# Kernel tuning notes

Measured on AMD Instinct MI355X. Metric: run time of the kernel, lower is better.

## Reference

```python
import jax, jax.numpy as jnp
import numpy as np

EMBED_DIM = 1024
SEQ_LEN = 4096
NUM_HEADS = 16
HEAD_DIM = EMBED_DIM // NUM_HEADS
FREQ_BINS = SEQ_LEN // 2 + 1  # 2049
LN_EPS = 1e-5


def setup_inputs() -> dict:
    key = jax.random.key(0)
    ks = jax.random.split(key, 12)
    B = 4
    x = jax.random.normal(ks[0], (B, SEQ_LEN, EMBED_DIM), dtype=jnp.float32)
    # LayerNorm affine params
    ln_w = jnp.ones((EMBED_DIM,), dtype=jnp.float32)
    ln_b = jnp.zeros((EMBED_DIM,), dtype=jnp.float32)
    # spectral base filter / bias: (H, freq_bins, 1)
    base_filter = jax.random.normal(ks[1], (NUM_HEADS, FREQ_BINS, 1), dtype=jnp.float32)
    base_bias = jax.random.normal(ks[2], (NUM_HEADS, FREQ_BINS, 1), dtype=jnp.float32) - 0.1
    # adaptive MLP (depth=2, width=embed_dim): D -> D -> D -> H*freq*2, relu hidden
    out_size = NUM_HEADS * FREQ_BINS * 2
    s0 = 1.0 / np.sqrt(EMBED_DIM)
    w0 = jax.random.uniform(ks[3], (EMBED_DIM, EMBED_DIM), jnp.float32, -s0, s0)
    b0 = jax.random.uniform(ks[4], (EMBED_DIM,), jnp.float32, -s0, s0)
    w1 = jax.random.uniform(ks[5], (EMBED_DIM, EMBED_DIM), jnp.float32, -s0, s0)
    b1 = jax.random.uniform(ks[6], (EMBED_DIM,), jnp.float32, -s0, s0)
    w2 = jax.random.uniform(ks[7], (EMBED_DIM, out_size), jnp.float32, -s0, s0)
    b2 = jax.random.uniform(ks[8], (out_size,), jnp.float32, -s0, s0)
    return {"x": x, "ln_w": ln_w, "ln_b": ln_b,
            "base_filter": base_filter, "base_bias": base_bias,
            "w0": w0, "b0": b0, "w1": w1, "b1": b1, "w2": w2, "b2": b2}


def _complex_activation(z):
    mag = jnp.abs(z)
    scale = jax.nn.gelu(mag) / (mag + 1e-6)
    return z * scale


def reference(x, ln_w, ln_b, base_filter, base_bias, w0, b0, w1, b1, w2, b2):
    B, N, D = x.shape  # N == SEQ_LEN, D == EMBED_DIM
    # pre-norm LayerNorm over last dim
    mu = x.mean(axis=-1, keepdims=True)
    var = x.var(axis=-1, keepdims=True)
    x_norm = (x - mu) / jnp.sqrt(var + LN_EPS) * ln_w + ln_b
    # split heads: (B, H, N, head_dim)
    x_heads = x_norm.reshape(B, N, NUM_HEADS, HEAD_DIM).transpose(0, 2, 1, 3)
    F_fft = jnp.fft.rfft(x_heads, axis=2)  # (B, H, freq, head_dim), complex
    # adaptive params from mean-pooled context
    context = x_norm.mean(axis=1)  # (B, D)
    h = jax.nn.relu(context @ w0 + b0)
    h = jax.nn.relu(h @ w1 + b1)
    adapt = h @ w2 + b2  # (B, H*freq*2)
    adapt = adapt.reshape(B, NUM_HEADS, FREQ_BINS, 2)
    adaptive_scale = adapt[..., 0:1]
    adaptive_bias = adapt[..., 1:2]
    effective_filter = base_filter * (1.0 + adaptive_scale)  # (B, H, freq, 1)
    effective_bias = base_bias + adaptive_bias
    F_mod = F_fft * effective_filter + effective_bias
    F_nl = _complex_activation(F_mod)
    x_filt = jnp.fft.irfft(F_nl, n=SEQ_LEN, axis=2)  # (B, H, N, head_dim)
    x_filt = x_filt.transpose(0, 2, 1, 3).reshape(B, SEQ_LEN, EMBED_DIM)
    return x_filt  # dropout is identity (inference / rate 0)
```

## Files before the change

kernel.cpp:

```cpp
#include <hip/hip_runtime.h>
#include <hip/hip_fp16.h>
#include <math.h>

#define B_ 4
#define N_ 4096
#define D_ 1024
#define H_ 16
#define HD_ 64
#define FB_ 2049

typedef unsigned short ushort_t;
typedef unsigned int uint_t;

__device__ __forceinline__ float2 cmul(float2 a, float2 b) {
    return make_float2(a.x*b.x - a.y*b.y, a.x*b.y + a.y*b.x);
}
__device__ __forceinline__ float2 cadd(float2 a, float2 b){return make_float2(a.x+b.x,a.y+b.y);}
__device__ __forceinline__ float2 csub(float2 a, float2 b){return make_float2(a.x-b.x,a.y-b.y);}
__device__ __forceinline__ float2 cconj(float2 a){return make_float2(a.x,-a.y);}
__device__ __forceinline__ float2 addi(float2 a, float2 b){return make_float2(a.x-b.y, a.y+b.x);}
__device__ __forceinline__ float2 subi(float2 a, float2 b){return make_float2(a.x+b.y, a.y-b.x);}

__device__ __forceinline__ float gelu_t(float m) {
    float u = 0.7978845608028654f * (m + 0.044715f * m * m * m);
    float e = __expf(-2.0f * u);
    float th = (1.0f - e) / (1.0f + e);
    return 0.5f * m * (1.0f + th);
}
__device__ __forceinline__ float2 cact(float2 z) {
    float m = sqrtf(z.x*z.x + z.y*z.y);
    float s = gelu_t(m) / (m + 1e-6f);
    return make_float2(z.x*s, z.y*s);
}

__device__ __forceinline__ ushort_t f2h(float f) {
    __half h = __float2half_rn(f);
    return *reinterpret_cast<ushort_t*>(&h);
}
__device__ __forceinline__ float h2f(ushort_t u) {
    __half h = *reinterpret_cast<__half*>(&u);
    return __half2float(h);
}
__device__ __forceinline__ uint_t pk2(float a, float b) {
    return (uint_t)f2h(a) | ((uint_t)f2h(b) << 16);
}
__device__ __forceinline__ float lo_f(uint_t u){ return h2f((ushort_t)(u & 0xffffu)); }
__device__ __forceinline__ float hi_f(uint_t u){ return h2f((ushort_t)(u >> 16)); }

#define IX(e) ((e) + ((e) >> 4))

__global__ __launch_bounds__(256) void k_normT(const float* __restrict__ x,
                                               const float* __restrict__ lnw,
                                               const float* __restrict__ lnb,
                                               ushort_t* __restrict__ xt,
                                               float* __restrict__ cpart) {
    __shared__ ushort_t lds16[32 * 1032];
    uint_t* lds32 = (uint_t*)lds16;
    int blk = blockIdx.x;
    int b = blk >> 7, chunk = blk & 127;
    int n0 = chunk << 5;
    int lane = threadIdx.x & 63, w = threadIdx.x >> 6;
    const float4* lw4 = (const float4*)lnw;
    const float4* lb4 = (const float4*)lnb;
    float4 W0 = lw4[lane], W1 = lw4[lane+64], W2 = lw4[lane+128], W3 = lw4[lane+192];
    float4 G0 = lb4[lane], G1 = lb4[lane+64], G2 = lb4[lane+128], G3 = lb4[lane+192];

    for (int j = 0; j < 8; j++) {
        int r = (w << 3) + j;
        const float4* xr = (const float4*)(x + ((size_t)b * N_ + n0 + r) * D_);
        float4 v0 = xr[lane], v1 = xr[lane+64], v2 = xr[lane+128], v3 = xr[lane+192];
        float s = v0.x+v0.y+v0.z+v0.w + v1.x+v1.y+v1.z+v1.w
                + v2.x+v2.y+v2.z+v2.w + v3.x+v3.y+v3.z+v3.w;
        float q = v0.x*v0.x+v0.y*v0.y+v0.z*v0.z+v0.w*v0.w
                + v1.x*v1.x+v1.y*v1.y+v1.z*v1.z+v1.w*v1.w
                + v2.x*v2.x+v2.y*v2.y+v2.z*v2.z+v2.w*v2.w
                + v3.x*v3.x+v3.y*v3.y+v3.z*v3.z+v3.w*v3.w;
        for (int o = 1; o < 64; o <<= 1) { s += __shfl_xor(s, o); q += __shfl_xor(q, o); }
        float mu = s * (1.0f / D_);
        float rstd = rsqrtf(q * (1.0f / D_) - mu * mu + 1e-5f);
        int base = r * 516 + 2 * lane;
        lds32[base]       = pk2((v0.x-mu)*rstd*W0.x+G0.x, (v0.y-mu)*rstd*W0.y+G0.y);
        lds32[base + 1]   = pk2((v0.z-mu)*rstd*W0.z+G0.z, (v0.w-mu)*rstd*W0.w+G0.w);
        lds32[base + 128] = pk2((v1.x-mu)*rstd*W1.x+G1.x, (v1.y-mu)*rstd*W1.y+G1.y);
        lds32[base + 129] = pk2((v1.z-mu)*rstd*W1.z+G1.z, (v1.w-mu)*rstd*W1.w+G1.w);
        lds32[base + 256] = pk2((v2.x-mu)*rstd*W2.x+G2.x, (v2.y-mu)*rstd*W2.y+G2.y);
        lds32[base + 257] = pk2((v2.z-mu)*rstd*W2.z+G2.z, (v2.w-mu)*rstd*W2.w+G2.w);
        lds32[base + 384] = pk2((v3.x-mu)*rstd*W3.x+G3.x, (v3.y-mu)*rstd*W3.y+G3.y);
        lds32[base + 385] = pk2((v3.z-mu)*rstd*W3.z+G3.z, (v3.w-mu)*rstd*W3.w+G3.w);
    }
    __syncthreads();
    for (int dd = 0; dd < 4; dd++) {
        int d = threadIdx.x + (dd << 8);
        float cs = 0.f;
        uint_t u[16];
        #pragma unroll
        for (int i = 0; i < 16; i++) {
            ushort_t h0 = lds16[(2*i) * 1032 + d];
            ushort_t h1 = lds16[(2*i+1) * 1032 + d];
            cs += h2f(h0) + h2f(h1);
            u[i] = (uint_t)h0 | ((uint_t)h1 << 16);
        }
        uint4* dst = (uint4*)(xt + ((size_t)(b * 1024 + d)) * 4096 + n0);
        dst[0] = make_uint4(u[0], u[1], u[2], u[3]);
        dst[1] = make_uint4(u[4], u[5], u[6], u[7]);
        dst[2] = make_uint4(u[8], u[9], u[10], u[11]);
        dst[3] = make_uint4(u[12], u[13], u[14], u[15]);
        cpart[((size_t)(b * 128 + chunk)) * D_ + d] = cs;
    }
}

__global__ __launch_bounds__(256) void k_ctx(const float* __restrict__ cpart,
                                             float* __restrict__ ctx) {
    int id = blockIdx.x * 256 + threadIdx.x;
    int b = id >> 10, d = id & 1023;
    float s = 0.f;
    const float* p = cpart + (size_t)b * 128 * D_ + d;
    #pragma unroll 8
    for (int g = 0; g < 128; g++) s += p[g * D_];
    ctx[id] = s * (1.0f / N_);
}

__global__ __launch_bounds__(256) void k_mlp_part(const float* __restrict__ in,
                                                  const float* __restrict__ w,
                                                  float* __restrict__ part) {
    __shared__ float li[4 * 256];
    int ks = blockIdx.y;
    for (int i = threadIdx.x; i < 1024; i += 256) {
        int b = i >> 8, kk = i & 255;
        li[i] = in[b * 1024 + ks * 256 + kk];
    }
    __syncthreads();
    int col = blockIdx.x * 64 + (threadIdx.x & 63);
    int b = threadIdx.x >> 6;
    const float* wp = w + (size_t)(ks * 256) * 1024 + col;
    const float* ip = li + b * 256;
    float acc = 0.f;
    #pragma unroll 8
    for (int k = 0; k < 256; k++) acc = fmaf(ip[k], wp[(size_t)k * 1024], acc);
    part[((size_t)ks * 4 + b) * 1024 + col] = acc;
}

__global__ __launch_bounds__(256) void k_mlp_part2(const float* __restrict__ part,
                                                   const float* __restrict__ bias,
                                                   const float* __restrict__ w,
                                                   float* __restrict__ part2) {
    __shared__ float li[4 * 256];
    int ks = blockIdx.y;
    for (int i = threadIdx.x; i < 1024; i += 256) {
        int b = i >> 8, kk = (i & 255) + ks * 256;
        float v = part[b * 1024 + kk] + part[4096 + b * 1024 + kk] +
                  part[8192 + b * 1024 + kk] + part[12288 + b * 1024 + kk] + bias[kk];
        li[i] = fmaxf(v, 0.f);
    }
    __syncthreads();
    int col = blockIdx.x * 64 + (threadIdx.x & 63);
    int b = threadIdx.x >> 6;
    const float* wp = w + (size_t)(ks * 256) * 1024 + col;
    const float* ip = li + b * 256;
    float acc = 0.f;
    #pragma unroll 8
    for (int k = 0; k < 256; k++) acc = fmaf(ip[k], wp[(size_t)k * 1024], acc);
    part2[((size_t)ks * 4 + b) * 1024 + col] = acc;
}

__global__ __launch_bounds__(256) void k_adapt_part(const float* __restrict__ part2,
                                                    const float* __restrict__ b1,
                                                    const float* __restrict__ w2,
                                                    float* __restrict__ part3) {
    __shared__ float lh[4 * 128];
    int ks = blockIdx.y;
    for (int i = threadIdx.x; i < 512; i += 256) {
        int b = i >> 7, kk = (i & 127) + ks * 128;
        float v = part2[b * 1024 + kk] + part2[4096 + b * 1024 + kk] +
                  part2[8192 + b * 1024 + kk] + part2[12288 + b * 1024 + kk] + b1[kk];
        lh[i] = fmaxf(v, 0.f);
    }
    __syncthreads();
    int j4 = blockIdx.x * 1024 + threadIdx.x * 4;
    if (j4 < 65568) {
        float a0x=0,a0y=0,a0z=0,a0w=0, a1x=0,a1y=0,a1z=0,a1w=0;
        float a2x=0,a2y=0,a2z=0,a2w=0, a3x=0,a3y=0,a3z=0,a3w=0;
        const float* wp = w2 + (size_t)(ks * 128) * 65568 + j4;
        #pragma unroll 4
        for (int k = 0; k < 128; k++) {
            float4 wv = *(const float4*)(wp + (size_t)k * 65568);
            float h0 = lh[k], h1 = lh[128 + k], h2 = lh[256 + k], h3 = lh[384 + k];
            a0x = fmaf(h0, wv.x, a0x); a0y = fmaf(h0, wv.y, a0y);
            a0z = fmaf(h0, wv.z, a0z); a0w = fmaf(h0, wv.w, a0w);
            a1x = fmaf(h1, wv.x, a1x); a1y = fmaf(h1, wv.y, a1y);
            a1z = fmaf(h1, wv.z, a1z); a1w = fmaf(h1, wv.w, a1w);
            a2x = fmaf(h2, wv.x, a2x); a2y = fmaf(h2, wv.y, a2y);
            a2z = fmaf(h2, wv.z, a2z); a2w = fmaf(h2, wv.w, a2w);
            a3x = fmaf(h3, wv.x, a3x); a3y = fmaf(h3, wv.y, a3y);
            a3z = fmaf(h3, wv.z, a3z); a3w = fmaf(h3, wv.w, a3w);
        }
        float* p3 = part3 + (size_t)ks * 4 * 65568 + j4;
        *(float4*)(p3)              = make_float4(a0x, a0y, a0z, a0w);
        *(float4*)(p3 + 65568)      = make_float4(a1x, a1y, a1z, a1w);
        *(float4*)(p3 + 2 * 65568)  = make_float4(a2x, a2y, a2z, a2w);
        *(float4*)(p3 + 3 * 65568)  = make_float4(a3x, a3y, a3z, a3w);
    }
}

__global__ __launch_bounds__(256) void k_eff(const float* __restrict__ part3,
                                             const float* __restrict__ b2,
                                             const float* __restrict__ bfilt,
                                             const float* __restrict__ bbias,
                                             float2* __restrict__ eff) {
    int p = blockIdx.x * 256 + threadIdx.x;
    if (p >= 32784) return;
    int h = p / 2049, f = p % 2049;
    float bf = bfilt[p], bb = bbias[p];
    float sc0 = b2[2 * p], bi0 = b2[2 * p + 1];
    #pragma unroll
    for (int b = 0; b < 4; b++) {
        float sc = sc0, bi = bi0;
        #pragma unroll
        for (int s = 0; s < 8; s++) {
            const float* q = part3 + ((size_t)s * 4 + b) * 65568 + 2 * p;
            sc += q[0]; bi += q[1];
        }
        eff[((size_t)b * H_ + h) * FB_ + f] = make_float2(bf * (1.0f + sc), bb + bi);
    }
}

__global__ __launch_bounds__(512) void k_fftmod(ushort_t* __restrict__ xt,
                                                const float2* __restrict__ eff) {
    __shared__ float2 bufA[4352];
    __shared__ float2 bufB[4352];
    __shared__ float2 tw[1088];
    const float s2 = 0.70710678118654752f;
    int t = threadIdx.x;
    int sig0 = blockIdx.x * 2;
    int b = sig0 >> 10;
    int h = (sig0 & 1023) >> 6;
    const float2* ef = eff + ((size_t)b * H_ + h) * FB_;
    ushort_t* xs = xt + (size_t)sig0 * 4096;

    #pragma unroll
    for (int ii = 0; ii < 2; ii++) {
        int ji = t + ii * 512;
        float sv, cv;
        __sincosf(-(float)M_PI * (float)ji * (1.0f / 2048.0f), &sv, &cv);
        tw[IX(ji)] = make_float2(cv, sv);
    }
    {
        const uint4* pa = (const uint4*)xs;
        const uint4* pb = pa + 512;
        uint4 ua = pa[t], ub = pb[t];
        int n = t << 3;
        bufA[IX(n+0)] = make_float2(lo_f(ua.x), lo_f(ub.x));
        bufA[IX(n+1)] = make_float2(hi_f(ua.x), hi_f(ub.x));
        bufA[IX(n+2)] = make_float2(lo_f(ua.y), lo_f(ub.y));
        bufA[IX(n+3)] = make_float2(hi_f(ua.y), hi_f(ub.y));
        bufA[IX(n+4)] = make_float2(lo_f(ua.z), lo_f(ub.z));
        bufA[IX(n+5)] = make_float2(hi_f(ua.z), hi_f(ub.z));
        bufA[IX(n+6)] = make_float2(lo_f(ua.w), lo_f(ub.w));
        bufA[IX(n+7)] = make_float2(hi_f(ua.w), hi_f(ub.w));
    }
    __syncthreads();

    float2 *src = bufA, *dst = bufB;
    for (int m = 1; m <= 512; m <<= 3) {
        int idx = t;
        int km = idx & (m - 1);
        int jm = idx - km;
        float2 u0 = src[IX(idx)];
        float2 u1 = src[IX(idx + 512)];
        float2 u2 = src[IX(idx + 1024)];
        float2 u3 = src[IX(idx + 1536)];
        float2 u4 = src[IX(idx + 2048)];
        float2 u5 = src[IX(idx + 2560)];
        float2 u6 = src[IX(idx + 3072)];
        float2 u7 = src[IX(idx + 3584)];
        float2 a0 = cadd(u0,u4), a1 = csub(u0,u4), a2 = cadd(u2,u6), a3 = csub(u2,u6);
        float2 E0 = cadd(a0,a2), E1 = subi(a1,a3), E2 = csub(a0,a2), E3 = addi(a1,a3);
        float2 c0 = cadd(u1,u5), c1 = csub(u1,u5), c2 = cadd(u3,u7), c3 = csub(u3,u7);
        float2 O0 = cadd(c0,c2), O1 = subi(c1,c3), O2 = csub(c0,c2), O3 = addi(c1,c3);
        float2 R1 = make_float2(s2*(O1.x + O1.y), s2*(O1.y - O1.x));
        float2 R2 = make_float2(O2.y, -O2.x);
        float2 R3 = make_float2(s2*(O3.y - O3.x), -s2*(O3.x + O3.y));
        float2 X0 = cadd(E0,O0), X4 = csub(E0,O0);
        float2 X1 = cadd(E1,R1), X5 = csub(E1,R1);
        float2 X2 = cadd(E2,R2), X6 = csub(E2,R2);
        float2 X3 = cadd(E3,R3), X7 = csub(E3,R3);
        float2 w1 = tw[IX(jm)];
        float2 w2 = cmul(w1,w1), w3 = cmul(w2,w1), w4 = cmul(w2,w2);
        float2 w5 = cmul(w4,w1), w6 = cmul(w4,w2), w7 = cmul(w4,w3);
        int base = 8*idx - 7*km;
        dst[IX(base)]       = X0;
        dst[IX(base + m)]   = cmul(w1,X1);
        dst[IX(base + 2*m)] = cmul(w2,X2);
        dst[IX(base + 3*m)] = cmul(w3,X3);
        dst[IX(base + 4*m)] = cmul(w4,X4);
        dst[IX(base + 5*m)] = cmul(w5,X5);
        dst[IX(base + 6*m)] = cmul(w6,X6);
        dst[IX(base + 7*m)] = cmul(w7,X7);
        __syncthreads();
        float2* tmp = src; src = dst; dst = tmp;
    }

    if (t == 0) {
        float2 Z = src[IX(0)];
        float2 e0 = ef[0];
        float Av = Z.x * e0.x + e0.y;
        float Bv = Z.y * e0.x + e0.y;
        float ma = fabsf(Av); Av *= gelu_t(ma) / (ma + 1e-6f);
        float mb = fabsf(Bv); Bv *= gelu_t(mb) / (mb + 1e-6f);
        dst[IX(0)] = make_float2(Av, Bv);
    }
    #pragma unroll
    for (int ii = 0; ii < 4; ii++) {
        int k = 1 + t + ii * 512;
        if (k == 2048) {
            float2 Z = src[IX(2048)];
            float2 eN = ef[2048];
            float Av = Z.x * eN.x + eN.y;
            float Bv = Z.y * eN.x + eN.y;
            float ma = fabsf(Av); Av *= gelu_t(ma) / (ma + 1e-6f);
            float mb = fabsf(Bv); Bv *= gelu_t(mb) / (mb + 1e-6f);
            dst[IX(2048)] = make_float2(Av, Bv);
        } else {
            float2 Zk = src[IX(k)], Zq = src[IX(4096 - k)];
            float2 A  = make_float2(0.5f*(Zk.x + Zq.x), 0.5f*(Zk.y - Zq.y));
            float2 Bc = make_float2(0.5f*(Zk.y + Zq.y), 0.5f*(Zq.x - Zk.x));
            float2 e = ef[k];
            float2 Ap = make_float2(A.x * e.x + e.y,  A.y * e.x);
            float2 Bp = make_float2(Bc.x * e.x + e.y, Bc.y * e.x);
            Ap = cact(Ap); Bp = cact(Bp);
            dst[IX(k)]        = make_float2(Ap.x - Bp.y, Ap.y + Bp.x);
            dst[IX(4096 - k)] = make_float2(Ap.x + Bp.y, Bp.x - Ap.y);
        }
    }
    __syncthreads();
    { float2* tmp = src; src = dst; dst = tmp; }

    for (int m = 1; m <= 512; m <<= 3) {
        int idx = t;
        int km = idx & (m - 1);
        int jm = idx - km;
        float2 u0 = src[IX(idx)];
        float2 u1 = src[IX(idx + 512)];
        float2 u2 = src[IX(idx + 1024)];
        float2 u3 = src[IX(idx + 1536)];
        float2 u4 = src[IX(idx + 2048)];
        float2 u5 = src[IX(idx + 2560)];
        float2 u6 = src[IX(idx + 3072)];
        float2 u7 = src[IX(idx + 3584)];
        float2 a0 = cadd(u0,u4), a1 = csub(u0,u4), a2 = cadd(u2,u6), a3 = csub(u2,u6);
        float2 E0 = cadd(a0,a2), E1 = addi(a1,a3), E2 = csub(a0,a2), E3 = subi(a1,a3);
        float2 c0 = cadd(u1,u5), c1 = csub(u1,u5), c2 = cadd(u3,u7), c3 = csub(u3,u7);
        float2 O0 = cadd(c0,c2), O1 = addi(c1,c3), O2 = csub(c0,c2), O3 = subi(c1,c3);
        float2 R1 = make_float2(s2*(O1.x - O1.y),  s2*(O1.x + O1.y));
        float2 R2 = make_float2(-O2.y, O2.x);
        float2 R3 = make_float2(-s2*(O3.x + O3.y), s2*(O3.x - O3.y));
        float2 X0 = cadd(E0,O0), X4 = csub(E0,O0);
        float2 X1 = cadd(E1,R1), X5 = csub(E1,R1);
        float2 X2 = cadd(E2,R2), X6 = csub(E2,R2);
        float2 X3 = cadd(E3,R3), X7 = csub(E3,R3);
        float2 w1 = cconj(tw[IX(jm)]);
        float2 w2 = cmul(w1,w1), w3 = cmul(w2,w1), w4 = cmul(w2,w2);
        float2 w5 = cmul(w4,w1), w6 = cmul(w4,w2), w7 = cmul(w4,w3);
        int base = 8*idx - 7*km;
        dst[IX(base)]       = X0;
        dst[IX(base + m)]   = cmul(w1,X1);
        dst[IX(base + 2*m)] = cmul(w2,X2);
        dst[IX(base + 3*m)] = cmul(w3,X3);
        dst[IX(base + 4*m)] = cmul(w4,X4);
        dst[IX(base + 5*m)] = cmul(w5,X5);
        dst[IX(base + 6*m)] = cmul(w6,X6);
        dst[IX(base + 7*m)] = cmul(w7,X7);
        __syncthreads();
        float2* tmp = src; src = dst; dst = tmp;
    }

    {
        const float sc = 1.0f / 4096.0f;
        int n = t << 3;
        float2 z0 = src[IX(n+0)], z1 = src[IX(n+1)], z2 = src[IX(n+2)], z3 = src[IX(n+3)];
        float2 z4 = src[IX(n+4)], z5 = src[IX(n+5)], z6 = src[IX(n+6)], z7 = src[IX(n+7)];
        uint4 oa, ob;
        oa.x = pk2(z0.x*sc, z1.x*sc); oa.y = pk2(z2.x*sc, z3.x*sc);
        oa.z = pk2(z4.x*sc, z5.x*sc); oa.w = pk2(z6.x*sc, z7.x*sc);
        ob.x = pk2(z0.y*sc, z1.y*sc); ob.y = pk2(z2.y*sc, z3.y*sc);
        ob.z = pk2(z4.y*sc, z5.y*sc); ob.w = pk2(z6.y*sc, z7.y*sc);
        ((uint4*)xs)[t] = oa;
        ((uint4*)xs)[t + 512] = ob;
    }
}

__global__ __launch_bounds__(256) void k_transout(const ushort_t* __restrict__ xt,
                                                  float* __restrict__ out) {
    __shared__ float tile[64 * 65];
    int bid = blockIdx.x;
    int b = bid >> 10;
    int rem = bid & 1023;
    int nt = rem >> 4;
    int dt = rem & 15;
    int n0 = nt << 6;
    int tx = threadIdx.x & 63, ty = threadIdx.x >> 6;
    const ushort_t* xtb = xt + ((size_t)((b * H_ + dt) * HD_)) * (size_t)N_ + n0;
    for (int r = 0; r < 16; r++) {
        int dloc = ty + 4 * r;
        tile[dloc * 65 + tx] = h2f(xtb[(size_t)dloc * N_ + tx]);
    }
    __syncthreads();
    float* ob = out + ((size_t)b * N_ + n0) * D_ + dt * HD_;
    for (int r = 0; r < 16; r++) {
        int nn = ty + 4 * r;
        ob[(size_t)nn * D_ + tx] = tile[tx * 65 + nn];
    }
}

extern "C" void kernel_launch(void* const* d_in, const int* in_sizes, int n_in,
                              void* d_out, int out_size, void* d_ws, size_t ws_size,
                              hipStream_t stream) {
    const float* x     = (const float*)d_in[0];
    const float* lnw   = (const float*)d_in[1];
    const float* lnb   = (const float*)d_in[2];
    const float* bfilt = (const float*)d_in[3];
    const float* bbias = (const float*)d_in[4];
    const float* w0    = (const float*)d_in[5];
    const float* b0    = (const float*)d_in[6];
    const float* w1    = (const float*)d_in[7];
    const float* b1    = (const float*)d_in[8];
    const float* w2    = (const float*)d_in[9];
    const float* b2    = (const float*)d_in[10];

    float* ws = (float*)d_ws;
    ushort_t* xt   = (ushort_t*)ws;
    float*  cpart  = ws + 8388608;
    float*  ctx    = ws + 8912896;
    float*  pA     = ws + 8916992;
    float*  pB     = ws + 8933376;
    float*  p3     = ws + 8949760;
    float2* eff    = (float2*)(ws + 11047936);
    float*  out    = (float*)d_out;

    k_normT     <<<512,  256, 0, stream>>>(x, lnw, lnb, xt, cpart);
    k_ctx       <<<16,   256, 0, stream>>>(cpart, ctx);
    k_mlp_part  <<<dim3(16, 4), 256, 0, stream>>>(ctx, w0, pA);
    k_mlp_part2 <<<dim3(16, 4), 256, 0, stream>>>(pA, b0, w1, pB);
    k_adapt_part<<<dim3(65, 8), 256, 0, stream>>>(pB, b1, w2, p3);
    k_eff       <<<129,  256, 0, stream>>>(p3, b2, bfilt, bbias, eff);
    k_fftmod    <<<2048, 512, 0, stream>>>(xt, eff);
    k_transout  <<<4096, 256, 0, stream>>>(xt, out);
}
```

Baseline: 227.4 us.

## Use in-place DIF/DIT FFT with digit-reversed spectrum and single LDS buffer

Replaces the ping-pong Stockham FFT with in-place decimation-in-frequency forward and decimation-in-time inverse radix-8 stages. The spectrum is left in digit-reversed order and the modulation step indexes it through rev12, so one LDS buffer is enough and the twiddle table is halved. The intent is to cut LDS use per block so more blocks fit per CU, with launch bounds now asking for 6 blocks per CU, and to skip twiddles in the trivial stage. The normT transpose also reads packed 32-bit LDS words and writes two columns per thread. Risks are bank conflicts from the strided in-place access and precision drift from computing twiddle powers by repeated multiplication.

```diff
diff --git a/kernel.cpp b/kernel.cpp
--- a/kernel.cpp
+++ b/kernel.cpp
@@ -48,6 +48,10 @@
 __device__ __forceinline__ float hi_f(uint_t u){ return h2f((ushort_t)(u >> 16)); }
 
 #define IX(e) ((e) + ((e) >> 4))
+
+__device__ __forceinline__ int rev12(int p) {
+    return ((p & 7) << 9) | (((p >> 3) & 7) << 6) | (((p >> 6) & 7) << 3) | ((p >> 9) & 7);
+}
 
 __global__ __launch_bounds__(256) void k_normT(const float* __restrict__ x,
                                                const float* __restrict__ lnw,
@@ -89,23 +93,31 @@
         lds32[base + 385] = pk2((v3.z-mu)*rstd*W3.z+G3.z, (v3.w-mu)*rstd*W3.w+G3.w);
     }
     __syncthreads();
-    for (int dd = 0; dd < 4; dd++) {
-        int d = threadIdx.x + (dd << 8);
-        float cs = 0.f;
-        uint_t u[16];
+    for (int half = 0; half < 2; half++) {
+        int dp = threadIdx.x + (half << 8);
+        float cs_e = 0.f, cs_o = 0.f;
+        uint_t ce[16], co[16];
         #pragma unroll
         for (int i = 0; i < 16; i++) {
-            ushort_t h0 = lds16[(2*i) * 1032 + d];
-            ushort_t h1 = lds16[(2*i+1) * 1032 + d];
-            cs += h2f(h0) + h2f(h1);
-            u[i] = (uint_t)h0 | ((uint_t)h1 << 16);
+            uint_t w0 = lds32[(2*i) * 516 + dp];
+            uint_t w1 = lds32[(2*i+1) * 516 + dp];
+            ce[i] = (w0 & 0xffffu) | (w1 << 16);
+            co[i] = (w0 >> 16) | (w1 & 0xffff0000u);
+            cs_e += lo_f(w0) + lo_f(w1);
+            cs_o += hi_f(w0) + hi_f(w1);
         }
-        uint4* dst = (uint4*)(xt + ((size_t)(b * 1024 + d)) * 4096 + n0);
-        dst[0] = make_uint4(u[0], u[1], u[2], u[3]);
-        dst[1] = make_uint4(u[4], u[5], u[6], u[7]);
-        dst[2] = make_uint4(u[8], u[9], u[10], u[11]);
-        dst[3] = make_uint4(u[12], u[13], u[14], u[15]);
-        cpart[((size_t)(b * 128 + chunk)) * D_ + d] = cs;
+        int de = dp * 2;
+        uint4* dste = (uint4*)(xt + ((size_t)(b * 1024 + de)) * 4096 + n0);
+        dste[0] = make_uint4(ce[0], ce[1], ce[2], ce[3]);
+        dste[1] = make_uint4(ce[4], ce[5], ce[6], ce[7]);
+        dste[2] = make_uint4(ce[8], ce[9], ce[10], ce[11]);
+        dste[3] = make_uint4(ce[12], ce[13], ce[14], ce[15]);
+        uint4* dsto = (uint4*)(xt + ((size_t)(b * 1024 + de + 1)) * 4096 + n0);
+        dsto[0] = make_uint4(co[0], co[1], co[2], co[3]);
+        dsto[1] = make_uint4(co[4], co[5], co[6], co[7]);
+        dsto[2] = make_uint4(co[8], co[9], co[10], co[11]);
+        dsto[3] = make_uint4(co[12], co[13], co[14], co[15]);
+        ((float2*)(cpart + ((size_t)(b * 128 + chunk)) * D_))[dp] = make_float2(cs_e, cs_o);
     }
 }
 
@@ -224,12 +236,99 @@
     }
 }
 
-__global__ __launch_bounds__(512) void k_fftmod(ushort_t* __restrict__ xt,
-                                                const float2* __restrict__ eff) {
-    __shared__ float2 bufA[4352];
-    __shared__ float2 bufB[4352];
-    __shared__ float2 tw[1088];
+template<int M, int SH, bool TW>
+__device__ __forceinline__ void dif_stage(float2* buf, const float2* tw, int t) {
     const float s2 = 0.70710678118654752f;
+    int j = t & (M - 1);
+    int base = 8 * t - 7 * j;
+    float2 u0 = buf[IX(base)];
+    float2 u1 = buf[IX(base + M)];
+    float2 u2 = buf[IX(base + 2*M)];
+    float2 u3 = buf[IX(base + 3*M)];
+    float2 u4 = buf[IX(base + 4*M)];
+    float2 u5 = buf[IX(base + 5*M)];
+    float2 u6 = buf[IX(base + 6*M)];
+    float2 u7 = buf[IX(base + 7*M)];
+    float2 a0 = cadd(u0,u4), a1 = csub(u0,u4), a2 = cadd(u2,u6), a3 = csub(u2,u6);
+    float2 E0 = cadd(a0,a2), E1 = subi(a1,a3), E2 = csub(a0,a2), E3 = addi(a1,a3);
+    float2 c0 = cadd(u1,u5), c1 = csub(u1,u5), c2 = cadd(u3,u7), c3 = csub(u3,u7);
+    float2 O0 = cadd(c0,c2), O1 = subi(c1,c3), O2 = csub(c0,c2), O3 = addi(c1,c3);
+    float2 R1 = make_float2(s2*(O1.x + O1.y), s2*(O1.y - O1.x));
+    float2 R2 = make_float2(O2.y, -O2.x);
+    float2 R3 = make_float2(s2*(O3.y - O3.x), -s2*(O3.x + O3.y));
+    float2 X0 = cadd(E0,O0), X4 = csub(E0,O0);
+    float2 X1 = cadd(E1,R1), X5 = csub(E1,R1);
+    float2 X2 = cadd(E2,R2), X6 = csub(E2,R2);
+    float2 X3 = cadd(E3,R3), X7 = csub(E3,R3);
+    buf[IX(base)] = X0;
+    if (TW) {
+        float2 w1 = tw[IX(j << SH)];
+        float2 w = w1;
+        buf[IX(base + M)]   = cmul(w, X1); w = cmul(w, w1);
+        buf[IX(base + 2*M)] = cmul(w, X2); w = cmul(w, w1);
+        buf[IX(base + 3*M)] = cmul(w, X3); w = cmul(w, w1);
+        buf[IX(base + 4*M)] = cmul(w, X4); w = cmul(w, w1);
+        buf[IX(base + 5*M)] = cmul(w, X5); w = cmul(w, w1);
+        buf[IX(base + 6*M)] = cmul(w, X6); w = cmul(w, w1);
+        buf[IX(base + 7*M)] = cmul(w, X7);
+    } else {
+        buf[IX(base + M)]   = X1;
+        buf[IX(base + 2*M)] = X2;
+        buf[IX(base + 3*M)] = X3;
+        buf[IX(base + 4*M)] = X4;
+        buf[IX(base + 5*M)] = X5;
+        buf[IX(base + 6*M)] = X6;
+        buf[IX(base + 7*M)] = X7;
+    }
+}
+
+template<int M, int SH, bool TW>
+__device__ __forceinline__ void dit_stage(float2* buf, const float2* tw, int t) {
+    const float s2 = 0.70710678118654752f;
+    int j = t & (M - 1);
+    int base = 8 * t - 7 * j;
+    float2 u0 = buf[IX(base)];
+    float2 u1, u2, u3, u4, u5, u6, u7;
+    if (TW) {
+        float2 w1 = cconj(tw[IX(j << SH)]);
+        float2 w = w1;
+        u1 = cmul(w, buf[IX(base + M)]);   w = cmul(w, w1);
+        u2 = cmul(w, buf[IX(base + 2*M)]); w = cmul(w, w1);
+        u3 = cmul(w, buf[IX(base + 3*M)]); w = cmul(w, w1);
+        u4 = cmul(w, buf[IX(base + 4*M)]); w = cmul(w, w1);
+        u5 = cmul(w, buf[IX(base + 5*M)]); w = cmul(w, w1);
+        u6 = cmul(w, buf[IX(base + 6*M)]); w = cmul(w, w1);
+        u7 = cmul(w, buf[IX(base + 7*M)]);
+    } else {
+        u1 = buf[IX(base + M)];
+        u2 = buf[IX(base + 2*M)];
+        u3 = buf[IX(base + 3*M)];
+        u4 = buf[IX(base + 4*M)];
+        u5 = buf[IX(base + 5*M)];
+        u6 = buf[IX(base + 6*M)];
+        u7 = buf[IX(base + 7*M)];
+    }
+    float2 a0 = cadd(u0,u4), a1 = csub(u0,u4), a2 = cadd(u2,u6), a3 = csub(u2,u6);
+    float2 E0 = cadd(a0,a2), E1 = addi(a1,a3), E2 = csub(a0,a2), E3 = subi(a1,a3);
+    float2 c0 = cadd(u1,u5), c1 = csub(u1,u5), c2 = cadd(u3,u7), c3 = csub(u3,u7);
+    float2 O0 = cadd(c0,c2), O1 = addi(c1,c3), O2 = csub(c0,c2), O3 = subi(c1,c3);
+    float2 R1 = make_float2(s2*(O1.x - O1.y),  s2*(O1.x + O1.y));
+    float2 R2 = make_float2(-O2.y, O2.x);
+    float2 R3 = make_float2(-s2*(O3.x + O3.y), s2*(O3.x - O3.y));
+    buf[IX(base)]       = cadd(E0,O0);
+    buf[IX(base + 4*M)] = csub(E0,O0);
+    buf[IX(base + M)]   = cadd(E1,R1);
+    buf[IX(base + 5*M)] = csub(E1,R1);
+    buf[IX(base + 2*M)] = cadd(E2,R2);
+    buf[IX(base + 6*M)] = csub(E2,R2);
+    buf[IX(base + 3*M)] = cadd(E3,R3);
+    buf[IX(base + 7*M)] = csub(E3,R3);
+}
+
+__global__ __launch_bounds__(512, 6) void k_fftmod(ushort_t* __restrict__ xt,
+                                                   const float2* __restrict__ eff) {
+    __shared__ float2 buf[4352];
+    __shared__ float2 tw[544];
     int t = threadIdx.x;
     int sig0 = blockIdx.x * 2;
     int b = sig0 >> 10;
@@ -237,148 +336,78 @@
     const float2* ef = eff + ((size_t)b * H_ + h) * FB_;
     ushort_t* xs = xt + (size_t)sig0 * 4096;
 
-    #pragma unroll
-    for (int ii = 0; ii < 2; ii++) {
-        int ji = t + ii * 512;
+    {
         float sv, cv;
-        __sincosf(-(float)M_PI * (float)ji * (1.0f / 2048.0f), &sv, &cv);
-        tw[IX(ji)] = make_float2(cv, sv);
+        __sincosf(-(float)M_PI * (float)t * (1.0f / 2048.0f), &sv, &cv);
+        tw[IX(t)] = make_float2(cv, sv);
     }
     {
         const uint4* pa = (const uint4*)xs;
         const uint4* pb = pa + 512;
         uint4 ua = pa[t], ub = pb[t];
         int n = t << 3;
-        bufA[IX(n+0)] = make_float2(lo_f(ua.x), lo_f(ub.x));
-        bufA[IX(n+1)] = make_float2(hi_f(ua.x), hi_f(ub.x));
-        bufA[IX(n+2)] = make_float2(lo_f(ua.y), lo_f(ub.y));
-        bufA[IX(n+3)] = make_float2(hi_f(ua.y), hi_f(ub.y));
-        bufA[IX(n+4)] = make_float2(lo_f(ua.z), lo_f(ub.z));
-        bufA[IX(n+5)] = make_float2(hi_f(ua.z), hi_f(ub.z));
-        bufA[IX(n+6)] = make_float2(lo_f(ua.w), lo_f(ub.w));
-        bufA[IX(n+7)] = make_float2(hi_f(ua.w), hi_f(ub.w));
-    }
-    __syncthreads();
-
-    float2 *src = bufA, *dst = bufB;
-    for (int m = 1; m <= 512; m <<= 3) {
-        int idx = t;
-        int km = idx & (m - 1);
-        int jm = idx - km;
-        float2 u0 = src[IX(idx)];
-        float2 u1 = src[IX(idx + 512)];
-        float2 u2 = src[IX(idx + 1024)];
-        float2 u3 = src[IX(idx + 1536)];
-        float2 u4 = src[IX(idx + 2048)];
-        float2 u5 = src[IX(idx + 2560)];
-        float2 u6 = src[IX(idx + 3072)];
-        float2 u7 = src[IX(idx + 3584)];
-        float2 a0 = cadd(u0,u4), a1 = csub(u0,u4), a2 = cadd(u2,u6), a3 = csub(u2,u6);
-        float2 E0 = cadd(a0,a2), E1 = subi(a1,a3), E2 = csub(a0,a2), E3 = addi(a1,a3);
-        float2 c0 = cadd(u1,u5), c1 = csub(u1,u5), c2 = cadd(u3,u7), c3 = csub(u3,u7);
-        float2 O0 = cadd(c0,c2), O1 = subi(c1,c3), O2 = csub(c0,c2), O3 = addi(c1,c3);
-        float2 R1 = make_float2(s2*(O1.x + O1.y), s2*(O1.y - O1.x));
-        float2 R2 = make_float2(O2.y, -O2.x);
-        float2 R3 = make_float2(s2*(O3.y - O3.x), -s2*(O3.x + O3.y));
-        float2 X0 = cadd(E0,O0), X4 = csub(E0,O0);
-        float2 X1 = cadd(E1,R1), X5 = csub(E1,R1);
-        float2 X2 = cadd(E2,R2), X6 = csub(E2,R2);
-        float2 X3 = cadd(E3,R3), X7 = csub(E3,R3);
-        float2 w1 = tw[IX(jm)];
-        float2 w2 = cmul(w1,w1), w3 = cmul(w2,w1), w4 = cmul(w2,w2);
-        float2 w5 = cmul(w4,w1), w6 = cmul(w4,w2), w7 = cmul(w4,w3);
-        int base = 8*idx - 7*km;
-        dst[IX(base)]       = X0;
-        dst[IX(base + m)]   = cmul(w1,X1);
-        dst[IX(base + 2*m)] = cmul(w2,X2);
-        dst[IX(base + 3*m)] = cmul(w3,X3);
-        dst[IX(base + 4*m)] = cmul(w4,X4);
-        dst[IX(base + 5*m)] = cmul(w5,X5);
-        dst[IX(base + 6*m)] = cmul(w6,X6);
-        dst[IX(base + 7*m)] = cmul(w7,X7);
-        __syncthreads();
-        float2* tmp = src; src = dst; dst = tmp;
-    }
+        buf[IX(n+0)] = make_float2(lo_f(ua.x), lo_f(ub.x));
+        buf[IX(n+1)] = make_float2(hi_f(ua.x), hi_f(ub.x));
+        buf[IX(n+2)] = make_float2(lo_f(ua.y), lo_f(ub.y));
+        buf[IX(n+3)] = make_float2(hi_f(ua.y), hi_f(ub.y));
+        buf[IX(n+4)] = make_float2(lo_f(ua.z), lo_f(ub.z));
+        buf[IX(n+5)] = make_float2(hi_f(ua.z), hi_f(ub.z));
+        buf[IX(n+6)] = make_float2(lo_f(ua.w), lo_f(ub.w));
+        buf[IX(n+7)] = make_float2(hi_f(ua.w), hi_f(ub.w));
+    }
+    __syncthreads();
+
+    dif_stage<512, 0, true >(buf, tw, t); __syncthreads();
+    dif_stage<64,  3, true >(buf, tw, t); __syncthreads();
+    dif_stage<8,   6, true >(buf, tw, t); __syncthreads();
+    dif_stage<1,   0, false>(buf, tw, t); __syncthreads();
 
     if (t == 0) {
-        float2 Z = src[IX(0)];
+        float2 Z = buf[IX(0)];
         float2 e0 = ef[0];
         float Av = Z.x * e0.x + e0.y;
         float Bv = Z.y * e0.x + e0.y;
         float ma = fabsf(Av); Av *= gelu_t(ma) / (ma + 1e-6f);
         float mb = fabsf(Bv); Bv *= gelu_t(mb) / (mb + 1e-6f);
-        dst[IX(0)] = make_float2(Av, Bv);
+        buf[IX(0)] = make_float2(Av, Bv);
     }
     #pragma unroll
     for (int ii = 0; ii < 4; ii++) {
-        int k = 1 + t + ii * 512;
+        int k = 1 + t + (ii << 9);
         if (k == 2048) {
-            float2 Z = src[IX(2048)];
+            float2 Z = buf[IX(4)];
             float2 eN = ef[2048];
             float Av = Z.x * eN.x + eN.y;
             float Bv = Z.y * eN.x + eN.y;
             float ma = fabsf(Av); Av *= gelu_t(ma) / (ma + 1e-6f);
             float mb = fabsf(Bv); Bv *= gelu_t(mb) / (mb + 1e-6f);
-            dst[IX(2048)] = make_float2(Av, Bv);
+            buf[IX(4)] = make_float2(Av, Bv);
         } else {
-            float2 Zk = src[IX(k)], Zq = src[IX(4096 - k)];
+            int pk = rev12(k);
+            int pq = rev12(4096 - k);
+            float2 Zk = buf[IX(pk)], Zq = buf[IX(pq)];
             float2 A  = make_float2(0.5f*(Zk.x + Zq.x), 0.5f*(Zk.y - Zq.y));
             float2 Bc = make_float2(0.5f*(Zk.y + Zq.y), 0.5f*(Zq.x - Zk.x));
             float2 e = ef[k];
             float2 Ap = make_float2(A.x * e.x + e.y,  A.y * e.x);
             float2 Bp = make_float2(Bc.x * e.x + e.y, Bc.y * e.x);
             Ap = cact(Ap); Bp = cact(Bp);
-            dst[IX(k)]        = make_float2(Ap.x - Bp.y, Ap.y + Bp.x);
-            dst[IX(4096 - k)] = make_float2(Ap.x + Bp.y, Bp.x - Ap.y);
+            buf[IX(pk)] = make_float2(Ap.x - Bp.y, Ap.y + Bp.x);
+            buf[IX(pq)] = make_float2(Ap.x + Bp.y, Bp.x - Ap.y);
         }
     }
     __syncthreads();
-    { float2* tmp = src; src = dst; dst = tmp; }
-
-    for (int m = 1; m <= 512; m <<= 3) {
-        int idx = t;
-        int km = idx & (m - 1);
-        int jm = idx - km;
-        float2 u0 = src[IX(idx)];
-        float2 u1 = src[IX(idx + 512)];
-        float2 u2 = src[IX(idx + 1024)];
-        float2 u3 = src[IX(idx + 1536)];
-        float2 u4 = src[IX(idx + 2048)];
-        float2 u5 = src[IX(idx + 2560)];
-        float2 u6 = src[IX(idx + 3072)];
-        float2 u7 = src[IX(idx + 3584)];
-        float2 a0 = cadd(u0,u4), a1 = csub(u0,u4), a2 = cadd(u2,u6), a3 = csub(u2,u6);
-        float2 E0 = cadd(a0,a2), E1 = addi(a1,a3), E2 = csub(a0,a2), E3 = subi(a1,a3);
-        float2 c0 = cadd(u1,u5), c1 = csub(u1,u5), c2 = cadd(u3,u7), c3 = csub(u3,u7);
-        float2 O0 = cadd(c0,c2), O1 = addi(c1,c3), O2 = csub(c0,c2), O3 = subi(c1,c3);
-        float2 R1 = make_float2(s2*(O1.x - O1.y),  s2*(O1.x + O1.y));
-        float2 R2 = make_float2(-O2.y, O2.x);
-        float2 R3 = make_float2(-s2*(O3.x + O3.y), s2*(O3.x - O3.y));
-        float2 X0 = cadd(E0,O0), X4 = csub(E0,O0);
-        float2 X1 = cadd(E1,R1), X5 = csub(E1,R1);
-        float2 X2 = cadd(E2,R2), X6 = csub(E2,R2);
-        float2 X3 = cadd(E3,R3), X7 = csub(E3,R3);
-        float2 w1 = cconj(tw[IX(jm)]);
-        float2 w2 = cmul(w1,w1), w3 = cmul(w2,w1), w4 = cmul(w2,w2);
-        float2 w5 = cmul(w4,w1), w6 = cmul(w4,w2), w7 = cmul(w4,w3);
-        int base = 8*idx - 7*km;
-        dst[IX(base)]       = X0;
-        dst[IX(base + m)]   = cmul(w1,X1);
-        dst[IX(base + 2*m)] = cmul(w2,X2);
-        dst[IX(base + 3*m)] = cmul(w3,X3);
-        dst[IX(base + 4*m)] = cmul(w4,X4);
-        dst[IX(base + 5*m)] = cmul(w5,X5);
-        dst[IX(base + 6*m)] = cmul(w6,X6);
-        dst[IX(base + 7*m)] = cmul(w7,X7);
-        __syncthreads();
-        float2* tmp = src; src = dst; dst = tmp;
-    }
+
+    dit_stage<1,   0, false>(buf, tw, t); __syncthreads();
+    dit_stage<8,   6, true >(buf, tw, t); __syncthreads();
+    dit_stage<64,  3, true >(buf, tw, t); __syncthreads();
+    dit_stage<512, 0, true >(buf, tw, t); __syncthreads();
 
     {
         const float sc = 1.0f / 4096.0f;
         int n = t << 3;
-        float2 z0 = src[IX(n+0)], z1 = src[IX(n+1)], z2 = src[IX(n+2)], z3 = src[IX(n+3)];
-        float2 z4 = src[IX(n+4)], z5 = src[IX(n+5)], z6 = src[IX(n+6)], z7 = src[IX(n+7)];
+        float2 z0 = buf[IX(n+0)], z1 = buf[IX(n+1)], z2 = buf[IX(n+2)], z3 = buf[IX(n+3)];
+        float2 z4 = buf[IX(n+4)], z5 = buf[IX(n+5)], z6 = buf[IX(n+6)], z7 = buf[IX(n+7)];
         uint4 oa, ob;
         oa.x = pk2(z0.x*sc, z1.x*sc); oa.y = pk2(z2.x*sc, z3.x*sc);
         oa.z = pk2(z4.x*sc, z5.x*sc); oa.w = pk2(z6.x*sc, z7.x*sc);
```

New measurement: 214.7 us. -5.6%, faster.
